# Performance work log

Measured on AMD Instinct MI355X. Metric: run time of the kernel, lower is better.

The kernel has to match this reference:

```python
import jax, jax.numpy as jnp
import numpy as np

# LocalConv config (must match init_kwargs)
B, C, H, W = 64, 16, 64, 64
KH, KW = 3, 3
SH, SW = 1, 1
OUT_CH = 32
OH = (H - KH + SH) // SH  # 62
OW = (W - KW + SW) // SW  # 62
P = OH * OW               # 3844 positions
FEAT = C * KH * KW        # 144 (flatten order: C, kh, kw)


def setup_inputs() -> dict:
    key = jax.random.key(0)
    k1, k2 = jax.random.split(key)
    inputs = jax.random.normal(k1, (B, C, H, W), dtype=jnp.float32)
    kernel = jax.random.normal(k2, (P, FEAT, OUT_CH), dtype=jnp.float32)
    return {"inputs": inputs, "kernel": kernel}


def _extract_patches(x):
    # x: (B, C, H, W) -> (P, B, FEAT) with FEAT flattened as (C, kh, kw),
    # matching torch's reshape of inputs[:, :, i:i+kh, j:j+kw].
    i_idx = (jnp.arange(OH) * SH)[:, None] + jnp.arange(KH)[None, :]  # (OH, KH)
    j_idx = (jnp.arange(OW) * SW)[:, None] + jnp.arange(KW)[None, :]  # (OW, KW)
    # gather -> (B, C, OH, KH, OW, KW)
    p = x[:, :, i_idx[:, :, None, None], j_idx[None, None, :, :]]
    # -> (OH, OW, B, C, KH, KW)
    p = jnp.transpose(p, (2, 4, 0, 1, 3, 5))
    return p.reshape(P, B, FEAT)


def reference(inputs, kernel):
    patches = _extract_patches(inputs)                 # (P, B, FEAT)
    out = jnp.einsum('pbf,pfo->pbo', patches, kernel)  # per-position unshared matmul
    out = out.reshape(OH, OW, B, OUT_CH)
    return jnp.transpose(out, (2, 3, 0, 1))            # (B, OUT_CH, OH, OW)
```

## Files before the change

kernel.cpp:

```cpp
#include <hip/hip_runtime.h>

#define CIN    16
#define HH     64
#define WW     64
#define OHD    62
#define OWD    62
#define OUTC   32
#define FEATN  144
#define POUT   (OHD*OWD)
#define LSTRB  152
#define AR_W   6
#define AR_ELEMS   (3*AR_W*64*16)
#define BBUF_ELEMS (OUTC*LSTRB + 8)

typedef __attribute__((ext_vector_type(8))) short  short8;
typedef __attribute__((ext_vector_type(4))) float  f32x4;
typedef __attribute__((ext_vector_type(4), aligned(4))) float f32x4u;
typedef __attribute__((ext_vector_type(2), aligned(4))) float f32x2u;

__device__ __forceinline__ unsigned short f2bf(float f) {
    unsigned int u = __float_as_uint(f);
    u += 0x7FFFu + ((u >> 16) & 1u);
    return (unsigned short)(u >> 16);
}

__device__ __forceinline__ void softBarrier() {
    asm volatile("s_waitcnt lgkmcnt(0)\n\ts_barrier" ::: "memory");
}

template<int TW>
__device__ __forceinline__ void conv_body(
    const float* __restrict__ inp, const float* __restrict__ wgt,
    float* __restrict__ out, int oh, int ow0,
    unsigned short* __restrict__ Araw, unsigned short* __restrict__ B_lds)
{
    const int tid = threadIdx.x;
    constexpr int WTOT = TW + 2;

    const int o_w = tid & 31;
    const int c_w = tid >> 5;
    const int p0  = oh * OWD + ow0;
    const float* wbase = wgt + (size_t)p0 * (FEATN * OUTC) + c_w * 288 + o_w;
    float ring[4][9];
    auto issue = [&](int t) {
        const float* p = wbase + (size_t)t * (FEATN * OUTC);
        #pragma unroll
        for (int g = 0; g < 9; ++g) ring[t & 3][g] = p[g * 32];
    };
    const int wb_base = o_w * LSTRB + c_w;
    auto writeB = [&](int t, unsigned short* Bb) {
        #pragma unroll
        for (int g = 0; g < 9; ++g)
            Bb[wb_base + g * 16] = f2bf(ring[t & 3][g]);
    };

    issue(0);
    if (TW > 1) issue(1);
    if (TW > 2) issue(2);
    if (TW > 3) issue(3);

    for (int t = tid; t < 3 * WTOT * 64; t += 512) {
        int w   = t % WTOT;
        int rem = t / WTOT;
        int b   = rem & 63;
        int kh  = rem >> 6;
        const float* src = inp + (size_t)b * (CIN * HH * WW)
                               + (size_t)(oh + kh) * WW + (ow0 + w);
        short8 h0, h1;
        #pragma unroll
        for (int c = 0; c < 8; ++c) h0[c] = (short)f2bf(src[c * (HH * WW)]);
        #pragma unroll
        for (int c = 0; c < 8; ++c) h1[c] = (short)f2bf(src[(c + 8) * (HH * WW)]);
        int s = (b >> 2) & 1;
        unsigned Gb = (unsigned)(((kh * AR_W + w) * 64 + b) * 2);
        unsigned wx = (unsigned)((w & 3) << 1);
        *(short8*)(Araw + (((Gb + s) ^ wx) << 3))       = h0;
        *(short8*)(Araw + (((Gb + (1 - s)) ^ wx) << 3)) = h1;
    }

    for (int t = tid; t < 2 * 264; t += 512) {
        int buf = t / 264, r = t % 264;
        int e = (r < 256) ? ((r >> 3) * LSTRB + 144 + (r & 7))
                          : (OUTC * LSTRB + (r & 7));
        B_lds[buf * BBUF_ELEMS + e] = 0;
    }

    writeB(0, B_lds);

    const int wid = tid >> 6, lane = tid & 63;
    const int fr = lane & 15, fq = lane >> 4, fqh = fq >> 1;
    const int mt = wid >> 1, nt = wid & 1;
    const int b  = mt * 16 + fr;
    const int gr = (fq & 1) ^ ((b >> 2) & 1);
    unsigned abase_g[5]; int kwv[5]; int boff[5];
    #pragma unroll
    for (int kc = 0; kc < 5; ++kc) {
        int g  = 2 * kc + fqh;
        int gc = (g > 8) ? 8 : g;
        int kh = (gc * 11) >> 5;
        int kw = gc - 3 * kh;
        abase_g[kc] = (unsigned)(((kh * AR_W + kw) * 64 + b) * 2 + gr);
        kwv[kc]     = kw;
        boff[kc]    = (nt * 16 + fr) * LSTRB + kc * 32 + fq * 8;
    }

    softBarrier();

    f32x4 acc[TW];
    #pragma unroll
    for (int q = 0; q < TW; ++q) acc[q] = (f32x4){0.f, 0.f, 0.f, 0.f};

    #pragma unroll
    for (int q = 0; q < TW; ++q) {
        const unsigned short* Bc = B_lds + (q & 1) * BBUF_ELEMS;
        #pragma unroll
        for (int kc = 0; kc < 5; ++kc) {
            short8 a;
            if (kc == 4 && fqh == 1) {
                a = (short8){0, 0, 0, 0, 0, 0, 0, 0};
            } else {
                unsigned gi = (abase_g[kc] + (unsigned)(q * 128))
                              ^ (unsigned)(((q + kwv[kc]) & 3) << 1);
                a = *(const short8*)(Araw + (gi << 3));
            }
            short8 bfv = *(const short8*)(Bc + boff[kc]);
            acc[q] = __builtin_amdgcn_mfma_f32_16x16x32_bf16(a, bfv, acc[q], 0, 0, 0);
        }
        if (q + 1 < TW) {
            writeB(q + 1, B_lds + ((q + 1) & 1) * BBUF_ELEMS);
            softBarrier();
        }
    }

    const int o = nt * 16 + fr;
    #pragma unroll
    for (int r = 0; r < 4; ++r) {
        float* dst = out + ((size_t)((mt * 16 + fq * 4 + r) * OUTC + o)) * POUT
                         + (size_t)oh * OWD + ow0;
        if constexpr (TW == 4) {
            f32x4u v = { acc[0][r], acc[1][r], acc[2][r], acc[3][r] };
            *(f32x4u*)dst = v;
        } else {
            f32x2u v = { acc[0][r], acc[1][r] };
            *(f32x2u*)dst = v;
        }
    }
}

__global__ __launch_bounds__(512, 4) void localconv_kernel(
    const float* __restrict__ inp,
    const float* __restrict__ wgt,
    float* __restrict__ out)
{
    __shared__ unsigned short Araw[AR_ELEMS];
    __shared__ unsigned short B_lds[2 * BBUF_ELEMS];

    const int bid = blockIdx.x;
    const int l   = (bid & 7) * 124 + (bid >> 3);
    const int oh    = l >> 4;
    const int strip = l & 15;

    if (strip < 15) conv_body<4>(inp, wgt, out, oh, strip * 4, Araw, B_lds);
    else            conv_body<2>(inp, wgt, out, oh, 60, Araw, B_lds);
}

extern "C" void kernel_launch(void* const* d_in, const int* in_sizes, int n_in,
                              void* d_out, int out_size, void* d_ws, size_t ws_size,
                              hipStream_t stream) {
    const float* inp = (const float*)d_in[0];
    const float* wgt = (const float*)d_in[1];
    float* out = (float*)d_out;
    localconv_kernel<<<dim3(992), 512, 0, stream>>>(inp, wgt, out);
}
```

Baseline: 43.93 us.

## Stage all weight tiles in LDS upfront and drop per-tile barriers

Replaces the double-buffered B tile in LDS, which was refilled between MFMA steps with a barrier each time, with TW separate buffers filled once before a single __syncthreads. All weight loads are converted and written up front, so the compute loop runs without intermediate barriers. LDS grows to four B buffers via dynamic shared memory, and launch bounds drop from 4 to 2 blocks per CU. This may lower occupancy and raise register pressure, since all weight values are held at once.

```diff
diff --git a/kernel.cpp b/kernel.cpp
--- a/kernel.cpp
+++ b/kernel.cpp
@@ -12,6 +12,7 @@
 #define AR_W   6
 #define AR_ELEMS   (3*AR_W*64*16)
 #define BBUF_ELEMS (OUTC*LSTRB + 8)
+#define SMEM_BYTES ((AR_ELEMS + 4*BBUF_ELEMS)*2)
 
 typedef __attribute__((ext_vector_type(8))) short  short8;
 typedef __attribute__((ext_vector_type(4))) float  f32x4;
@@ -22,10 +23,6 @@
     unsigned int u = __float_as_uint(f);
     u += 0x7FFFu + ((u >> 16) & 1u);
     return (unsigned short)(u >> 16);
-}
-
-__device__ __forceinline__ void softBarrier() {
-    asm volatile("s_waitcnt lgkmcnt(0)\n\ts_barrier" ::: "memory");
 }
 
 template<int TW>
@@ -41,23 +38,13 @@
     const int c_w = tid >> 5;
     const int p0  = oh * OWD + ow0;
     const float* wbase = wgt + (size_t)p0 * (FEATN * OUTC) + c_w * 288 + o_w;
-    float ring[4][9];
-    auto issue = [&](int t) {
-        const float* p = wbase + (size_t)t * (FEATN * OUTC);
+    float wv[TW][9];
+    #pragma unroll
+    for (int q = 0; q < TW; ++q) {
+        const float* p = wbase + (size_t)q * (FEATN * OUTC);
         #pragma unroll
-        for (int g = 0; g < 9; ++g) ring[t & 3][g] = p[g * 32];
-    };
-    const int wb_base = o_w * LSTRB + c_w;
-    auto writeB = [&](int t, unsigned short* Bb) {
-        #pragma unroll
-        for (int g = 0; g < 9; ++g)
-            Bb[wb_base + g * 16] = f2bf(ring[t & 3][g]);
-    };
-
-    issue(0);
-    if (TW > 1) issue(1);
-    if (TW > 2) issue(2);
-    if (TW > 3) issue(3);
+        for (int g = 0; g < 9; ++g) wv[q][g] = p[g * 32];
+    }
 
     for (int t = tid; t < 3 * WTOT * 64; t += 512) {
         int w   = t % WTOT;
@@ -78,14 +65,21 @@
         *(short8*)(Araw + (((Gb + (1 - s)) ^ wx) << 3)) = h1;
     }
 
-    for (int t = tid; t < 2 * 264; t += 512) {
+    for (int t = tid; t < TW * 264; t += 512) {
         int buf = t / 264, r = t % 264;
         int e = (r < 256) ? ((r >> 3) * LSTRB + 144 + (r & 7))
                           : (OUTC * LSTRB + (r & 7));
         B_lds[buf * BBUF_ELEMS + e] = 0;
     }
 
-    writeB(0, B_lds);
+    const int wb_base = o_w * LSTRB + c_w;
+    #pragma unroll
+    for (int q = 0; q < TW; ++q) {
+        unsigned short* Bb = B_lds + q * BBUF_ELEMS;
+        #pragma unroll
+        for (int g = 0; g < 9; ++g)
+            Bb[wb_base + g * 16] = f2bf(wv[q][g]);
+    }
 
     const int wid = tid >> 6, lane = tid & 63;
     const int fr = lane & 15, fq = lane >> 4, fqh = fq >> 1;
@@ -104,7 +98,7 @@
         boff[kc]    = (nt * 16 + fr) * LSTRB + kc * 32 + fq * 8;
     }
 
-    softBarrier();
+    __syncthreads();
 
     f32x4 acc[TW];
     #pragma unroll
@@ -112,7 +106,7 @@
 
     #pragma unroll
     for (int q = 0; q < TW; ++q) {
-        const unsigned short* Bc = B_lds + (q & 1) * BBUF_ELEMS;
+        const unsigned short* Bc = B_lds + q * BBUF_ELEMS;
         #pragma unroll
         for (int kc = 0; kc < 5; ++kc) {
             short8 a;
@@ -125,10 +119,6 @@
             }
             short8 bfv = *(const short8*)(Bc + boff[kc]);
             acc[q] = __builtin_amdgcn_mfma_f32_16x16x32_bf16(a, bfv, acc[q], 0, 0, 0);
-        }
-        if (q + 1 < TW) {
-            writeB(q + 1, B_lds + ((q + 1) & 1) * BBUF_ELEMS);
-            softBarrier();
         }
     }
 
@@ -147,13 +137,14 @@
     }
 }
 
-__global__ __launch_bounds__(512, 4) void localconv_kernel(
+__global__ __launch_bounds__(512, 2) void localconv_kernel(
     const float* __restrict__ inp,
     const float* __restrict__ wgt,
     float* __restrict__ out)
 {
-    __shared__ unsigned short Araw[AR_ELEMS];
-    __shared__ unsigned short B_lds[2 * BBUF_ELEMS];
+    extern __shared__ unsigned short smem[];
+    unsigned short* Araw  = smem;
+    unsigned short* B_lds = smem + AR_ELEMS;
 
     const int bid = blockIdx.x;
     const int l   = (bid & 7) * 124 + (bid >> 3);
@@ -170,5 +161,7 @@
     const float* inp = (const float*)d_in[0];
     const float* wgt = (const float*)d_in[1];
     float* out = (float*)d_out;
-    localconv_kernel<<<dim3(992), 512, 0, stream>>>(inp, wgt, out);
+    hipFuncSetAttribute((const void*)localconv_kernel,
+                        hipFuncAttributeMaxDynamicSharedMemorySize, SMEM_BYTES);
+    localconv_kernel<<<dim3(992), 512, SMEM_BYTES, stream>>>(inp, wgt, out);
 }
```

New measurement: 42.89 us. -2.4%, faster.
